# Optimization experiments

Hardware: AMD Instinct MI355X
Metric: run time of the kernel (lower is better)

Reference implementation:

```python
import jax, jax.numpy as jnp
import numpy as np

EMBED_DIM = 1024
NUM_HEADS = 16
HEAD_DIM = EMBED_DIM // NUM_HEADS


def setup_inputs() -> dict:
    key = jax.random.key(0)
    k_x, k_wqkv, k_bqkv, k_wo, k_bo = jax.random.split(key, 5)
    B, T, C = 4, 2048, EMBED_DIM
    bound = 1.0 / np.sqrt(C)
    return {
        "x": jax.random.normal(k_x, (B, T, C), dtype=jnp.float32),
        "w_qkv": jax.random.uniform(k_wqkv, (C, 3 * C), jnp.float32, -bound, bound),
        "b_qkv": jax.random.uniform(k_bqkv, (3 * C,), jnp.float32, -bound, bound),
        "w_out": jax.random.uniform(k_wo, (C, C), jnp.float32, -bound, bound),
        "b_out": jax.random.uniform(k_bo, (C,), jnp.float32, -bound, bound),
    }


def reference(x, w_qkv, b_qkv, w_out, b_out):
    B, T, C = x.shape
    H, D = NUM_HEADS, HEAD_DIM
    qkv = x @ w_qkv + b_qkv                       # [B,T,3C]
    qkv = qkv.reshape(B, T, 3, H, D)
    q, k, v = qkv[:, :, 0], qkv[:, :, 1], qkv[:, :, 2]  # [B,T,H,D]
    scale = 1.0 / np.sqrt(D).astype(np.float32)
    scores = jnp.einsum("bqhd,bkhd->bhqk", q, k) * scale  # [B,H,T,T]
    causal = jnp.tril(jnp.ones((T, T), dtype=bool))
    scores = jnp.where(causal, scores, -jnp.inf)
    attn = jax.nn.softmax(scores, axis=-1)
    # dropout p=0.0 / eval mode -> identity
    ctx = jnp.einsum("bhqk,bkhd->bqhd", attn, v).reshape(B, T, C)
    return ctx @ w_out + b_out
```

## Files before the change

kernel.cpp:

```cpp
#include <hip/hip_runtime.h>
#include <hip/hip_bf16.h>

#define NB 4
#define NT 2048
#define NC 1024
#define NH 16
#define ND 64
#define BT (NB*NT)
#define LOG2E 1.4426950408889634f
#define NEG_BIG (-3.0e38f)
#define MLC 28.853900817779268f

typedef __attribute__((ext_vector_type(8))) short bf16x8;
typedef __attribute__((ext_vector_type(4))) float f32x4;

static __device__ __forceinline__ short f2bf(float f) {
    union { float f; unsigned u; } v; v.f = f;
    unsigned r = (v.u + 0x7fffu + ((v.u >> 16) & 1u)) >> 16;
    return (short)r;
}

static __device__ __forceinline__ unsigned pk2(float a, float b) {
#if __has_builtin(__builtin_amdgcn_cvt_pk_bf16_f32)
    auto v = __builtin_amdgcn_cvt_pk_bf16_f32(a, b);
    union { decltype(v) v; unsigned u; } c; c.v = v; return c.u;
#else
    return (unsigned)(unsigned short)f2bf(a) | ((unsigned)(unsigned short)f2bf(b) << 16);
#endif
}

static __device__ __forceinline__ f32x4 mfma16(bf16x8 a, bf16x8 b, f32x4 c) {
    return __builtin_amdgcn_mfma_f32_16x16x32_bf16(a, b, c, 0, 0, 0);
}

static __device__ __forceinline__ float fexp2(float x) {
#if __has_builtin(__builtin_amdgcn_exp2f)
    return __builtin_amdgcn_exp2f(x);
#else
    return exp2f(x);
#endif
}

template<int GOFF>
static __device__ __forceinline__ void gload_lds16(const short* g, short* l) {
    __builtin_amdgcn_global_load_lds(
        (const __attribute__((address_space(1))) void*)g,
        (__attribute__((address_space(3))) void*)l,
        16, GOFF, 0);
}

static __device__ __forceinline__ void transpose_body(
    const float* __restrict__ w, short* __restrict__ wt, int R, int Cn,
    int bx, int by, int tid, short (*t)[72])
{
    const int r0 = bx * 64;
    const int c0 = by * 64;
    {
        const int rl = tid >> 2, c4 = (tid & 3) << 4;
        const float* src = w + (size_t)(r0 + rl) * Cn + c0 + c4;
        float4 f0 = *(const float4*)(src + 0);
        float4 f1 = *(const float4*)(src + 4);
        float4 f2 = *(const float4*)(src + 8);
        float4 f3 = *(const float4*)(src + 12);
        short* d = &t[rl][c4];
        d[0]=f2bf(f0.x); d[1]=f2bf(f0.y); d[2]=f2bf(f0.z); d[3]=f2bf(f0.w);
        d[4]=f2bf(f1.x); d[5]=f2bf(f1.y); d[6]=f2bf(f1.z); d[7]=f2bf(f1.w);
        d[8]=f2bf(f2.x); d[9]=f2bf(f2.y); d[10]=f2bf(f2.z); d[11]=f2bf(f2.w);
        d[12]=f2bf(f3.x); d[13]=f2bf(f3.y); d[14]=f2bf(f3.z); d[15]=f2bf(f3.w);
    }
    __syncthreads();
    {
        const int cl = tid >> 2, r4 = (tid & 3) << 4;
        bf16x8 p0, p1;
#pragma unroll
        for (int j = 0; j < 8; ++j) { p0[j] = t[r4 + j][cl]; p1[j] = t[r4 + 8 + j][cl]; }
        short* dst = wt + (size_t)(c0 + cl) * R + r0 + r4;
        *(bf16x8*)dst       = p0;
        *(bf16x8*)(dst + 8) = p1;
    }
}

__global__ __launch_bounds__(256)
void prep(const float* __restrict__ x, short* __restrict__ xb,
          const float* __restrict__ wq, short* __restrict__ wtq,
          const float* __restrict__ wo, short* __restrict__ wto)
{
    __shared__ short t[64][72];
    const int bid = blockIdx.x;
    const int tid = threadIdx.x;
    if (bid < 4096) {
        const size_t i = ((size_t)bid * 256 + tid) * 8;
        float4 f0 = *(const float4*)(x + i);
        float4 f1 = *(const float4*)(x + i + 4);
        uint4 p;
        p.x = pk2(f0.x, f0.y); p.y = pk2(f0.z, f0.w);
        p.z = pk2(f1.x, f1.y); p.w = pk2(f1.z, f1.w);
        *(uint4*)(xb + i) = p;
    } else if (bid < 4096 + 768) {
        const int idx = bid - 4096;
        transpose_body(wq, wtq, NC, 3*NC, idx & 15, idx >> 4, tid, t);
    } else {
        const int idx = bid - (4096 + 768);
        transpose_body(wo, wto, NC, NC, idx & 15, idx >> 4, tid, t);
    }
}

__global__ __launch_bounds__(256)
void transpose_w(const float* __restrict__ w, short* __restrict__ wt, int R, int Cn)
{
    __shared__ short t[64][72];
    transpose_body(w, wt, R, Cn, blockIdx.x, blockIdx.y, threadIdx.x, t);
}

__global__ __launch_bounds__(512, 2)
void qkv_gemm8(const short* __restrict__ xb, const short* __restrict__ wt,
               const float* __restrict__ bias,
               short* __restrict__ q, short* __restrict__ k, short* __restrict__ vt)
{
    __shared__ short aLds[3][256 * 64];
    __shared__ short bLds[3][128 * 64];
    const int tid  = threadIdx.x;
    const int lane = tid & 63;
    const int wave = tid >> 6;
    const int waveM = wave & 3;
    const int waveN = wave >> 2;
    const int quad = lane >> 4;
    const int l15  = lane & 15;
    const int l7   = l15 & 7;
    const int m0 = blockIdx.x * 256;
    const int n0 = blockIdx.y * 128;

    const int rsub = lane >> 3;
    const int gcol = ((lane & 7) ^ rsub) * 8;

    f32x4 acc[4][4];
#pragma unroll
    for (int i = 0; i < 4; ++i)
#pragma unroll
        for (int j = 0; j < 4; ++j) acc[i][j] = 0.0f;

    bf16x8 aF[4][2];
    bf16x8 bF[2][2][2];

    auto stA = [&](int bufi, int kt) {
#pragma unroll
        for (int c = 0; c < 4; ++c) {
            const int rb = c*64 + wave*8;
            gload_lds16<0>(xb + (size_t)(m0 + rb + rsub) * NC + kt*64 + gcol,
                           &aLds[bufi][rb * 64]);
        }
    };
    auto stB = [&](int bufi, int kt) {
#pragma unroll
        for (int c = 0; c < 2; ++c) {
            const int rb = c*64 + wave*8;
            gload_lds16<0>(wt + (size_t)(n0 + rb + rsub) * NC + kt*64 + gcol,
                           &bLds[bufi][rb * 64]);
        }
    };
    auto rdA = [&](int bufi) {
#pragma unroll
        for (int mi = 0; mi < 4; ++mi)
#pragma unroll
            for (int kd = 0; kd < 2; ++kd) {
                const int r = waveM*64 + mi*16 + l15;
                aF[mi][kd] = *(const bf16x8*)
                    &aLds[bufi][r*64 + (((kd*4 + quad) ^ l7) * 8)];
            }
    };
    auto rdB = [&](int bufi, int nh) {
#pragma unroll
        for (int ni = 0; ni < 2; ++ni)
#pragma unroll
            for (int kd = 0; kd < 2; ++kd) {
                const int r = waveN*64 + nh*32 + ni*16 + l15;
                bF[nh][ni][kd] = *(const bf16x8*)
                    &bLds[bufi][r*64 + (((kd*4 + quad) ^ l7) * 8)];
            }
    };
    auto mm32 = [&]() {
        __builtin_amdgcn_s_setprio(1);
#pragma unroll
        for (int nh = 0; nh < 2; ++nh)
#pragma unroll
            for (int mi = 0; mi < 4; ++mi)
#pragma unroll
                for (int ni = 0; ni < 2; ++ni) {
                    f32x4 c = acc[mi][nh*2 + ni];
                    c = mfma16(aF[mi][0], bF[nh][ni][0], c);
                    c = mfma16(aF[mi][1], bF[nh][ni][1], c);
                    acc[mi][nh*2 + ni] = c;
                }
        __builtin_amdgcn_s_setprio(0);
    };

    stA(0, 0); stB(0, 0);
    stA(1, 1); stB(1, 1);
    asm volatile("s_waitcnt vmcnt(6)" ::: "memory");
    __builtin_amdgcn_s_barrier();

    int cur = 0;
#pragma unroll 1
    for (int kt = 0; kt < 16; ++kt) {
        const int stg = (cur >= 1) ? cur - 1 : 2;
        rdA(cur); rdB(cur, 0); rdB(cur, 1);
        if (kt + 2 < 16) { stA(stg, kt + 2); stB(stg, kt + 2); }
        asm volatile("s_waitcnt lgkmcnt(0)" ::: "memory");
        __builtin_amdgcn_sched_barrier(0);
        mm32();
        if (kt + 2 < 16)      asm volatile("s_waitcnt vmcnt(6)" ::: "memory");
        else if (kt + 1 < 16) asm volatile("s_waitcnt vmcnt(0)" ::: "memory");
        __builtin_amdgcn_s_barrier();
        cur = (cur == 2) ? 0 : cur + 1;
    }

#pragma unroll
    for (int mi = 0; mi < 4; ++mi) {
#pragma unroll
        for (int nj = 0; nj < 4; ++nj) {
            const int n = n0 + waveN*64 + nj*16 + l15;
            const float bb = bias[n];
            const int s = n >> 10;
            const int h = (n >> 6) & 15;
            const int d = n & 63;
#pragma unroll
            for (int r = 0; r < 4; ++r) {
                const int m = m0 + waveM*64 + mi*16 + quad*4 + r;
                const int b = m >> 11;
                const int t = m & (NT - 1);
                const float val = acc[mi][nj][r] + bb;
                const size_t bhx = (size_t)(b * NH + h);
                if (s == 0)      q [(bhx * NT + t) * ND + d] = f2bf(val * 0.125f);
                else if (s == 1) k [(bhx * NT + t) * ND + d] = f2bf(val);
                else             vt[(bhx * ND + d) * NT + t] = f2bf(val);
            }
        }
    }
}

__global__ __launch_bounds__(256)
void attn(const short* __restrict__ q, const short* __restrict__ k,
          const short* __restrict__ vt, short* __restrict__ ctx)
{
    __shared__ short kbuf[2][128 * 64];
    __shared__ short vbuf[2][64 * 128];
    __shared__ short pbuf[4][32 * 64];
    const int tid  = threadIdx.x;
    const int lane = tid & 63;
    const int wave = tid >> 6;
    const int quad = lane >> 4;
    const int l15  = lane & 15;
    const int l7   = l15 & 7;
    const int bh = blockIdx.x;
    const int b  = bh >> 4;
    const int h  = bh & 15;

    const short* Qp = q  + (size_t)bh * NT * ND;
    const short* Kp = k  + (size_t)bh * NT * ND;
    const short* Vp = vt + (size_t)bh * ND * NT;

    const int srowK   = lane >> 3;
    const int schunkK = ((lane & 7) ^ srowK) * 8;
    const int srowV   = lane >> 4;
    short* pw = &pbuf[wave][0];

    bf16x8 ones;
#pragma unroll
    for (int j = 0; j < 8; ++j) ones[j] = (short)0x3F80;

    const int qblock = 15 - (int)blockIdx.y;
    const int qb  = qblock * 128;
    const int wq0 = qb + wave * 32;
    const int ktB = qblock + 1;

    bf16x8 qf[2][2];
#pragma unroll
    for (int mi = 0; mi < 2; ++mi)
#pragma unroll
        for (int kd = 0; kd < 2; ++kd)
            qf[mi][kd] = *(const bf16x8*)(Qp + (size_t)(wq0 + mi*16 + l15) * ND + kd*32 + quad*8);

    f32x4 ot[4][2];
    f32x4 la[2];
#pragma unroll
    for (int di = 0; di < 4; ++di)
#pragma unroll
        for (int mi = 0; mi < 2; ++mi) ot[di][mi] = 0.0f;
    la[0] = 0.0f; la[1] = 0.0f;

    auto stKV = [&](int p, int kb) {
#pragma unroll
        for (int i = 0; i < 4; ++i) {
            const int r = wave*32 + i*8;
            gload_lds16<0>(Kp + (size_t)(kb + r + srowK) * ND + schunkK,
                           &kbuf[p][r * 64]);
        }
#pragma unroll
        for (int i = 0; i < 4; ++i) {
            const int r = wave*16 + i*4;
            const int rr = r + srowV;
            const int cc = ((lane & 15) ^ (rr & 7)) * 8;
            gload_lds16<0>(Vp + (size_t)rr * NT + kb + cc,
                           &vbuf[p][r * 128]);
        }
    };

    stKV(0, 0);

    for (int kt = 0; kt < ktB; ++kt) {
        const int p  = kt & 1;
        const int kb = kt << 7;
        __syncthreads();

        if (kt + 1 < ktB) stKV(1 - p, kb + 128);

#pragma unroll
        for (int hf = 0; hf < 2; ++hf) {
            const int kbh = kb + hf*64;
            if (kbh > wq0 + 31) continue;

            bf16x8 kf[4][2];
#pragma unroll
            for (int ni = 0; ni < 4; ++ni)
#pragma unroll
                for (int kd = 0; kd < 2; ++kd)
                    kf[ni][kd] = *(const bf16x8*)
                        &kbuf[p][(hf*64 + ni*16 + l15)*64 + (((kd*4 + quad) ^ l7) * 8)];

            f32x4 st[4][2];
#pragma unroll
            for (int ni = 0; ni < 4; ++ni)
#pragma unroll
                for (int mi = 0; mi < 2; ++mi) {
                    st[ni][mi] = 0.0f;
                    st[ni][mi] = mfma16(kf[ni][0], qf[mi][0], st[ni][mi]);
                    st[ni][mi] = mfma16(kf[ni][1], qf[mi][1], st[ni][mi]);
                }

            if (kbh + 63 > wq0) {
#pragma unroll
                for (int ni = 0; ni < 4; ++ni)
#pragma unroll
                    for (int mi = 0; mi < 2; ++mi) {
                        const int qrow = wq0 + mi*16 + l15;
#pragma unroll
                        for (int r = 0; r < 4; ++r) {
                            const int key = kbh + ni*16 + quad*4 + r;
                            if (key > qrow) st[ni][mi][r] = NEG_BIG;
                        }
                    }
            }

#pragma unroll
            for (int mi = 0; mi < 2; ++mi) {
#pragma unroll
                for (int ni = 0; ni < 4; ++ni) {
#pragma unroll
                    for (int r = 0; r < 4; ++r)
                        st[ni][mi][r] = fexp2(fmaf(st[ni][mi][r], LOG2E, -MLC));
                    const f32x4 v = st[ni][mi];
                    *(uint2*)&pw[(mi*16 + l15)*64
                                 + (((2*ni + (quad >> 1)) ^ l7) * 8)
                                 + (quad & 1) * 4] =
                        make_uint2(pk2(v[0], v[1]), pk2(v[2], v[3]));
                }
            }

            bf16x8 vf[4][2], pf[2][2];
#pragma unroll
            for (int di = 0; di < 4; ++di)
#pragma unroll
                for (int kd = 0; kd < 2; ++kd)
                    vf[di][kd] = *(const bf16x8*)
                        &vbuf[p][(di*16 + l15)*128
                                 + (hf*8 + ((kd*4 + quad) ^ l7)) * 8];
#pragma unroll
            for (int mi = 0; mi < 2; ++mi)
#pragma unroll
                for (int kd = 0; kd < 2; ++kd)
                    pf[mi][kd] = *(const bf16x8*)
                        &pw[(mi*16 + l15)*64 + (((kd*4 + quad) ^ l7) * 8)];

#pragma unroll
            for (int mi = 0; mi < 2; ++mi) {
                la[mi] = mfma16(ones, pf[mi][0], la[mi]);
                la[mi] = mfma16(ones, pf[mi][1], la[mi]);
            }

#pragma unroll
            for (int di = 0; di < 4; ++di)
#pragma unroll
                for (int mi = 0; mi < 2; ++mi) {
                    ot[di][mi] = mfma16(vf[di][0], pf[mi][0], ot[di][mi]);
                    ot[di][mi] = mfma16(vf[di][1], pf[mi][1], ot[di][mi]);
                }
        }
    }

#pragma unroll
    for (int mi = 0; mi < 2; ++mi) {
        const float inv = 1.0f / la[mi][0];
        const int t = wq0 + mi*16 + l15;
        short* dst = ctx + ((size_t)(b * NT + t)) * NC + h*64 + quad*4;
#pragma unroll
        for (int di = 0; di < 4; ++di) {
            const f32x4 v = ot[di][mi] * inv;
            *(uint2*)(dst + di*16) = make_uint2(pk2(v[0], v[1]), pk2(v[2], v[3]));
        }
    }
}

__global__ __launch_bounds__(512, 2)
void out_gemm8(const short* __restrict__ a, const short* __restrict__ wt,
               const float* __restrict__ bias, float* __restrict__ out)
{
    __shared__ short aLds[3][256 * 64];
    __shared__ short bLds[3][128 * 64];
    const int tid  = threadIdx.x;
    const int lane = tid & 63;
    const int wave = tid >> 6;
    const int waveM = wave & 3;
    const int waveN = wave >> 2;
    const int quad = lane >> 4;
    const int l15  = lane & 15;
    const int l7   = l15 & 7;
    const int m0 = blockIdx.x * 256;
    const int n0 = blockIdx.y * 128;

    const int rsub = lane >> 3;
    const int gcol = ((lane & 7) ^ rsub) * 8;

    f32x4 acc[4][4];
#pragma unroll
    for (int i = 0; i < 4; ++i)
#pragma unroll
        for (int j = 0; j < 4; ++j) acc[i][j] = 0.0f;

    bf16x8 aF[4][2];
    bf16x8 bF[2][2][2];

    auto stA = [&](int bufi, int kt) {
#pragma unroll
        for (int c = 0; c < 4; ++c) {
            const int rb = c*64 + wave*8;
            gload_lds16<0>(a + (size_t)(m0 + rb + rsub) * NC + kt*64 + gcol,
                           &aLds[bufi][rb * 64]);
        }
    };
    auto stB = [&](int bufi, int kt) {
#pragma unroll
        for (int c = 0; c < 2; ++c) {
            const int rb = c*64 + wave*8;
            gload_lds16<0>(wt + (size_t)(n0 + rb + rsub) * NC + kt*64 + gcol,
                           &bLds[bufi][rb * 64]);
        }
    };
    auto rdA = [&](int bufi) {
#pragma unroll
        for (int mi = 0; mi < 4; ++mi)
#pragma unroll
            for (int kd = 0; kd < 2; ++kd) {
                const int r = waveM*64 + mi*16 + l15;
                aF[mi][kd] = *(const bf16x8*)
                    &aLds[bufi][r*64 + (((kd*4 + quad) ^ l7) * 8)];
            }
    };
    auto rdB = [&](int bufi, int nh) {
#pragma unroll
        for (int ni = 0; ni < 2; ++ni)
#pragma unroll
            for (int kd = 0; kd < 2; ++kd) {
                const int r = waveN*64 + nh*32 + ni*16 + l15;
                bF[nh][ni][kd] = *(const bf16x8*)
                    &bLds[bufi][r*64 + (((kd*4 + quad) ^ l7) * 8)];
            }
    };
    auto mm32 = [&]() {
        __builtin_amdgcn_s_setprio(1);
#pragma unroll
        for (int nh = 0; nh < 2; ++nh)
#pragma unroll
            for (int mi = 0; mi < 4; ++mi)
#pragma unroll
                for (int ni = 0; ni < 2; ++ni) {
                    f32x4 c = acc[mi][nh*2 + ni];
                    c = mfma16(aF[mi][0], bF[nh][ni][0], c);
                    c = mfma16(aF[mi][1], bF[nh][ni][1], c);
                    acc[mi][nh*2 + ni] = c;
                }
        __builtin_amdgcn_s_setprio(0);
    };

    stA(0, 0); stB(0, 0);
    stA(1, 1); stB(1, 1);
    asm volatile("s_waitcnt vmcnt(6)" ::: "memory");
    __builtin_amdgcn_s_barrier();

    int cur = 0;
#pragma unroll 1
    for (int kt = 0; kt < 16; ++kt) {
        const int stg = (cur >= 1) ? cur - 1 : 2;
        rdA(cur); rdB(cur, 0); rdB(cur, 1);
        if (kt + 2 < 16) { stA(stg, kt + 2); stB(stg, kt + 2); }
        asm volatile("s_waitcnt lgkmcnt(0)" ::: "memory");
        __builtin_amdgcn_sched_barrier(0);
        mm32();
        if (kt + 2 < 16)      asm volatile("s_waitcnt vmcnt(6)" ::: "memory");
        else if (kt + 1 < 16) asm volatile("s_waitcnt vmcnt(0)" ::: "memory");
        __builtin_amdgcn_s_barrier();
        cur = (cur == 2) ? 0 : cur + 1;
    }

#pragma unroll
    for (int mi = 0; mi < 4; ++mi) {
#pragma unroll
        for (int nj = 0; nj < 4; ++nj) {
            const int n = n0 + waveN*64 + nj*16 + l15;
            const float bb = bias[n];
#pragma unroll
            for (int r = 0; r < 4; ++r) {
                const int m = m0 + waveM*64 + mi*16 + quad*4 + r;
                out[(size_t)m * NC + n] = acc[mi][nj][r] + bb;
            }
        }
    }
}

extern "C" void kernel_launch(void* const* d_in, const int* in_sizes, int n_in,
                              void* d_out, int out_size, void* d_ws, size_t ws_size,
                              hipStream_t stream)
{
    const float* x     = (const float*)d_in[0];
    const float* w_qkv = (const float*)d_in[1];
    const float* b_qkv = (const float*)d_in[2];
    const float* w_out = (const float*)d_in[3];
    const float* b_out = (const float*)d_in[4];
    float* out = (float*)d_out;

    const size_t SZ = (size_t)NB * NH * NT * ND;
    short* q   = (short*)d_ws;
    short* kk  = q  + SZ;
    short* vt  = kk + SZ;
    short* ctx = vt + SZ;
    short* xbf = ctx + SZ;
    short* wTq = ctx;

    const size_t need = 5 * SZ * 2 + (size_t)NC * NC * 2;
    const int hoist = (ws_size >= need);
    short* wTo = hoist ? (xbf + SZ) : xbf;

    const int prepBlocks = 4096 + 768 + (hoist ? 256 : 0);
    hipLaunchKernelGGL(prep, dim3(prepBlocks), dim3(256), 0, stream,
                       x, xbf, w_qkv, wTq, w_out, wTo);
    hipLaunchKernelGGL(qkv_gemm8, dim3(BT/256, (3*NC)/128), dim3(512), 0, stream,
                       xbf, wTq, b_qkv, q, kk, vt);
    hipLaunchKernelGGL(attn, dim3(NB*NH, 16), dim3(256), 0, stream,
                       q, kk, vt, ctx);
    if (!hoist)
        hipLaunchKernelGGL(transpose_w, dim3(16, 16), dim3(256), 0, stream,
                           w_out, wTo, NC, NC);
    hipLaunchKernelGGL(out_gemm8, dim3(BT/256, NC/128), dim3(512), 0, stream,
                       ctx, wTo, b_out, out);
}
```

Measured before the change: 250.5 us.

## Restructure attention to 256-row query blocks with 64-key tiles and 8 waves

The attention kernel now runs 512 threads (8 waves) per block, each block covering 256 query rows, and streams 64-key K/V tiles instead of 128-key tiles split into halves. Each staged K/V tile is now shared by twice as many query rows, which cuts global and LDS staging traffic per query. In exchange the grid has half as many blocks, causal load imbalance per block grows, and the number of barriers per block goes up because tiles are smaller. The launch bound asks for 4 blocks per CU, which limits registers per thread.

```diff
diff --git a/kernel.cpp b/kernel.cpp
--- a/kernel.cpp
+++ b/kernel.cpp
@@ -238,13 +238,13 @@
     }
 }
 
-__global__ __launch_bounds__(256)
+__global__ __launch_bounds__(512, 4)
 void attn(const short* __restrict__ q, const short* __restrict__ k,
           const short* __restrict__ vt, short* __restrict__ ctx)
 {
-    __shared__ short kbuf[2][128 * 64];
-    __shared__ short vbuf[2][64 * 128];
-    __shared__ short pbuf[4][32 * 64];
+    __shared__ short kbuf[2][64 * 64];
+    __shared__ short vbuf[2][64 * 64];
+    __shared__ short pbuf[8][32 * 64];
     const int tid  = threadIdx.x;
     const int lane = tid & 63;
     const int wave = tid >> 6;
@@ -261,17 +261,16 @@
 
     const int srowK   = lane >> 3;
     const int schunkK = ((lane & 7) ^ srowK) * 8;
-    const int srowV   = lane >> 4;
     short* pw = &pbuf[wave][0];
 
     bf16x8 ones;
 #pragma unroll
     for (int j = 0; j < 8; ++j) ones[j] = (short)0x3F80;
 
-    const int qblock = 15 - (int)blockIdx.y;
-    const int qb  = qblock * 128;
+    const int qblock = 7 - (int)blockIdx.y;
+    const int qb  = qblock * 256;
     const int wq0 = qb + wave * 32;
-    const int ktB = qblock + 1;
+    const int ktB = qblock * 4 + 4;
 
     bf16x8 qf[2][2];
 #pragma unroll
@@ -289,112 +288,98 @@
     la[0] = 0.0f; la[1] = 0.0f;
 
     auto stKV = [&](int p, int kb) {
-#pragma unroll
-        for (int i = 0; i < 4; ++i) {
-            const int r = wave*32 + i*8;
-            gload_lds16<0>(Kp + (size_t)(kb + r + srowK) * ND + schunkK,
-                           &kbuf[p][r * 64]);
-        }
-#pragma unroll
-        for (int i = 0; i < 4; ++i) {
-            const int r = wave*16 + i*4;
-            const int rr = r + srowV;
-            const int cc = ((lane & 15) ^ (rr & 7)) * 8;
-            gload_lds16<0>(Vp + (size_t)rr * NT + kb + cc,
-                           &vbuf[p][r * 128]);
-        }
+        const int r = wave * 8;
+        gload_lds16<0>(Kp + (size_t)(kb + r + srowK) * ND + schunkK,
+                       &kbuf[p][r * 64]);
+        gload_lds16<0>(Vp + (size_t)(r + srowK) * NT + kb + schunkK,
+                       &vbuf[p][r * 64]);
     };
 
     stKV(0, 0);
 
     for (int kt = 0; kt < ktB; ++kt) {
         const int p  = kt & 1;
-        const int kb = kt << 7;
+        const int kb = kt << 6;
         __syncthreads();
 
-        if (kt + 1 < ktB) stKV(1 - p, kb + 128);
-
-#pragma unroll
-        for (int hf = 0; hf < 2; ++hf) {
-            const int kbh = kb + hf*64;
-            if (kbh > wq0 + 31) continue;
-
-            bf16x8 kf[4][2];
+        if (kt + 1 < ktB) stKV(1 - p, kb + 64);
+
+        if (kb > wq0 + 31) continue;
+
+        bf16x8 kf[4][2];
+#pragma unroll
+        for (int ni = 0; ni < 4; ++ni)
+#pragma unroll
+            for (int kd = 0; kd < 2; ++kd)
+                kf[ni][kd] = *(const bf16x8*)
+                    &kbuf[p][(ni*16 + l15)*64 + (((kd*4 + quad) ^ l7) * 8)];
+
+        f32x4 st[4][2];
+#pragma unroll
+        for (int ni = 0; ni < 4; ++ni)
+#pragma unroll
+            for (int mi = 0; mi < 2; ++mi) {
+                st[ni][mi] = 0.0f;
+                st[ni][mi] = mfma16(kf[ni][0], qf[mi][0], st[ni][mi]);
+                st[ni][mi] = mfma16(kf[ni][1], qf[mi][1], st[ni][mi]);
+            }
+
+        if (kb + 63 > wq0) {
 #pragma unroll
             for (int ni = 0; ni < 4; ++ni)
 #pragma unroll
-                for (int kd = 0; kd < 2; ++kd)
-                    kf[ni][kd] = *(const bf16x8*)
-                        &kbuf[p][(hf*64 + ni*16 + l15)*64 + (((kd*4 + quad) ^ l7) * 8)];
-
-            f32x4 st[4][2];
-#pragma unroll
-            for (int ni = 0; ni < 4; ++ni)
-#pragma unroll
                 for (int mi = 0; mi < 2; ++mi) {
-                    st[ni][mi] = 0.0f;
-                    st[ni][mi] = mfma16(kf[ni][0], qf[mi][0], st[ni][mi]);
-                    st[ni][mi] = mfma16(kf[ni][1], qf[mi][1], st[ni][mi]);
+                    const int qrow = wq0 + mi*16 + l15;
+#pragma unroll
+                    for (int r = 0; r < 4; ++r) {
+                        const int key = kb + ni*16 + quad*4 + r;
+                        if (key > qrow) st[ni][mi][r] = NEG_BIG;
+                    }
                 }
-
-            if (kbh + 63 > wq0) {
-#pragma unroll
-                for (int ni = 0; ni < 4; ++ni)
-#pragma unroll
-                    for (int mi = 0; mi < 2; ++mi) {
-                        const int qrow = wq0 + mi*16 + l15;
-#pragma unroll
-                        for (int r = 0; r < 4; ++r) {
-                            const int key = kbh + ni*16 + quad*4 + r;
-                            if (key > qrow) st[ni][mi][r] = NEG_BIG;
-                        }
-                    }
-            }
-
+        }
+
+#pragma unroll
+        for (int mi = 0; mi < 2; ++mi) {
+#pragma unroll
+            for (int ni = 0; ni < 4; ++ni) {
+#pragma unroll
+                for (int r = 0; r < 4; ++r)
+                    st[ni][mi][r] = fexp2(fmaf(st[ni][mi][r], LOG2E, -MLC));
+                const f32x4 v = st[ni][mi];
+                *(uint2*)&pw[(mi*16 + l15)*64
+                             + (((2*ni + (quad >> 1)) ^ l7) * 8)
+                             + (quad & 1) * 4] =
+                    make_uint2(pk2(v[0], v[1]), pk2(v[2], v[3]));
+            }
+        }
+
+        bf16x8 vf[4][2], pf[2][2];
+#pragma unroll
+        for (int di = 0; di < 4; ++di)
+#pragma unroll
+            for (int kd = 0; kd < 2; ++kd)
+                vf[di][kd] = *(const bf16x8*)
+                    &vbuf[p][(di*16 + l15)*64 + (((kd*4 + quad) ^ l7) * 8)];
+#pragma unroll
+        for (int mi = 0; mi < 2; ++mi)
+#pragma unroll
+            for (int kd = 0; kd < 2; ++kd)
+                pf[mi][kd] = *(const bf16x8*)
+                    &pw[(mi*16 + l15)*64 + (((kd*4 + quad) ^ l7) * 8)];
+
+#pragma unroll
+        for (int mi = 0; mi < 2; ++mi) {
+            la[mi] = mfma16(ones, pf[mi][0], la[mi]);
+            la[mi] = mfma16(ones, pf[mi][1], la[mi]);
+        }
+
+#pragma unroll
+        for (int di = 0; di < 4; ++di)
 #pragma unroll
             for (int mi = 0; mi < 2; ++mi) {
-#pragma unroll
-                for (int ni = 0; ni < 4; ++ni) {
-#pragma unroll
-                    for (int r = 0; r < 4; ++r)
-                        st[ni][mi][r] = fexp2(fmaf(st[ni][mi][r], LOG2E, -MLC));
-                    const f32x4 v = st[ni][mi];
-                    *(uint2*)&pw[(mi*16 + l15)*64
-                                 + (((2*ni + (quad >> 1)) ^ l7) * 8)
-                                 + (quad & 1) * 4] =
-                        make_uint2(pk2(v[0], v[1]), pk2(v[2], v[3]));
-                }
-            }
-
-            bf16x8 vf[4][2], pf[2][2];
-#pragma unroll
-            for (int di = 0; di < 4; ++di)
-#pragma unroll
-                for (int kd = 0; kd < 2; ++kd)
-                    vf[di][kd] = *(const bf16x8*)
-                        &vbuf[p][(di*16 + l15)*128
-                                 + (hf*8 + ((kd*4 + quad) ^ l7)) * 8];
-#pragma unroll
-            for (int mi = 0; mi < 2; ++mi)
-#pragma unroll
-                for (int kd = 0; kd < 2; ++kd)
-                    pf[mi][kd] = *(const bf16x8*)
-                        &pw[(mi*16 + l15)*64 + (((kd*4 + quad) ^ l7) * 8)];
-
-#pragma unroll
-            for (int mi = 0; mi < 2; ++mi) {
-                la[mi] = mfma16(ones, pf[mi][0], la[mi]);
-                la[mi] = mfma16(ones, pf[mi][1], la[mi]);
-            }
-
-#pragma unroll
-            for (int di = 0; di < 4; ++di)
-#pragma unroll
-                for (int mi = 0; mi < 2; ++mi) {
-                    ot[di][mi] = mfma16(vf[di][0], pf[mi][0], ot[di][mi]);
-                    ot[di][mi] = mfma16(vf[di][1], pf[mi][1], ot[di][mi]);
-                }
-        }
+                ot[di][mi] = mfma16(vf[di][0], pf[mi][0], ot[di][mi]);
+                ot[di][mi] = mfma16(vf[di][1], pf[mi][1], ot[di][mi]);
+            }
     }
 
 #pragma unroll
@@ -554,7 +539,7 @@
                        x, xbf, w_qkv, wTq, w_out, wTo);
     hipLaunchKernelGGL(qkv_gemm8, dim3(BT/256, (3*NC)/128), dim3(512), 0, stream,
                        xbf, wTq, b_qkv, q, kk, vt);
-    hipLaunchKernelGGL(attn, dim3(NB*NH, 16), dim3(256), 0, stream,
+    hipLaunchKernelGGL(attn, dim3(NB*NH, 8), dim3(512), 0, stream,
                        q, kk, vt, ctx);
     if (!hoist)
         hipLaunchKernelGGL(transpose_w, dim3(16, 16), dim3(256), 0, stream,
```

New measurement: 254.8 us. Within noise of the previous version (+1.7%).
